# Kernel tuning notes

Hardware: AMD Instinct MI355X
Metric: run time of the kernel (lower is better)

## Reference

```python
import jax, jax.numpy as jnp
import numpy as np

N_NODES = 50000
N_EDGES = 1600000
NODE_DIM = 64
HID = 16


def setup_inputs() -> dict:
    key = jax.random.key(0)
    ks = jax.random.split(key, 12)
    f = lambda k, shape: (jax.random.normal(k, shape, dtype=jnp.float32) * 0.1)
    edge_index = jax.random.randint(ks[0], (2, N_EDGES), 0, N_NODES)
    return {
        "edge_index": edge_index,
        "node_emb": f(ks[1], (N_NODES, NODE_DIM)),
        "edge_emb": f(ks[2], (N_EDGES, HID)),
        "W1": f(ks[3], (NODE_DIM, HID)),
        "att_src1": f(ks[4], (HID,)),
        "att_dst1": f(ks[5], (HID,)),
        "b1": jnp.zeros((HID,), jnp.float32),
        "W2": f(ks[6], (HID, HID)),
        "att_src2": f(ks[7], (HID,)),
        "att_dst2": f(ks[8], (HID,)),
        "b2": jnp.zeros((HID,), jnp.float32),
        "Wm1": f(ks[9], (3 * HID, HID)),
        "bm1": jnp.zeros((HID,), jnp.float32),
        "Wm2": f(ks[10], (HID, 1)),
        "bm2": jnp.zeros((1,), jnp.float32),
    }


def gat_layer(x, src, dst, W, a_src, a_dst, b, num_nodes):
    # Single-head GATConv (PyG defaults): self-loops, leaky_relu(0.2), softmax over dst.
    h = x @ W  # [N, out]
    logits = jax.nn.leaky_relu((h @ a_src)[src] + (h @ a_dst)[dst], negative_slope=0.2)
    m = jax.ops.segment_max(logits, dst, num_segments=num_nodes)  # stable softmax
    e = jnp.exp(logits - jax.lax.stop_gradient(m)[dst])
    denom = jax.ops.segment_sum(e, dst, num_segments=num_nodes)
    coef = e / denom[dst]  # [E+N]
    out = jax.ops.segment_sum(coef[:, None] * h[src], dst, num_segments=num_nodes)
    return out + b


def reference(edge_index, node_emb, edge_emb, W1, att_src1, att_dst1, b1,
              W2, att_src2, att_dst2, b2, Wm1, bm1, Wm2, bm2):
    src, dst = edge_index[0], edge_index[1]
    num_nodes = node_emb.shape[0]
    loops = jnp.arange(num_nodes)
    src_f = jnp.concatenate([src, loops])  # GATConv add_self_loops=True
    dst_f = jnp.concatenate([dst, loops])

    x = node_emb
    for (W, a_s, a_d, b) in [(W1, att_src1, att_dst1, b1), (W2, att_src2, att_dst2, b2)]:
        x = gat_layer(x, src_f, dst_f, W, a_s, a_d, b, num_nodes)
        x = jax.nn.gelu(x, approximate=False)  # torch F.gelu default = exact erf
        # dropout omitted (eval mode)

    # Vectorized replacement of the per-edge Python loop:
    edge_repr = jnp.concatenate([x[src], x[dst], edge_emb], axis=1)  # [E, 3*HID]
    hmid = jax.nn.relu(edge_repr @ Wm1 + bm1)
    probs = jax.nn.sigmoid(hmid @ Wm2 + bm2)[:, 0]  # [E]
    return probs
```

## Files before the change

### kernel.cpp

```cpp
#include <hip/hip_runtime.h>
#include <math.h>

#define N_NODES 50000
#define N_EDGES 1600000
#define NODE_DIM 64
#define HID 16
#define BSZ 64
#define NBUCK ((N_NODES + BSZ - 1) / BSZ)
#define CAPB 2560
#define EPB 2048
#define APB 256
#define APPEND_BLOCKS ((N_EDGES + EPB - 1) / EPB)

typedef _Float16 h8 __attribute__((ext_vector_type(8)));

__global__ void append_kernel(const int* __restrict__ ei,
                              int* __restrict__ gcount,
                              unsigned int* __restrict__ blist) {
    __shared__ int lcount[NBUCK];
    __shared__ int gbase[NBUCK];
    __shared__ int loff[NBUCK];
    int t = threadIdx.x;
    for (int b = t; b < NBUCK; b += APB) { lcount[b] = 0; loff[b] = 0; }
    __syncthreads();
    long base = (long)blockIdx.x * EPB;
#pragma unroll
    for (int k = 0; k < EPB / APB; k++) {
        long i = base + k * APB + t;
        if (i < N_EDGES) atomicAdd(&lcount[ei[N_EDGES + i] >> 6], 1);
    }
    __syncthreads();
    for (int b = t; b < NBUCK; b += APB) {
        int c = lcount[b];
        gbase[b] = c ? atomicAdd(&gcount[b], c) : 0;
    }
    __syncthreads();
#pragma unroll
    for (int k = 0; k < EPB / APB; k++) {
        long i = base + k * APB + t;
        if (i < N_EDGES) {
            int s = ei[i], d = ei[N_EDGES + i];
            int b = d >> 6;
            int pos = gbase[b] + atomicAdd(&loff[b], 1);
            if (pos < CAPB)
                blist[(size_t)b * CAPB + pos] = ((unsigned)(d & 63) << 16) | (unsigned)s;
        }
    }
}

__global__ void sort_kernel(const int* __restrict__ gcount, const unsigned int* __restrict__ blist,
                            unsigned short* __restrict__ csr, int* __restrict__ dstbeg) {
    __shared__ int cnts[BSZ];
    __shared__ int sc[BSZ];
    __shared__ int off[BSZ];
    int b = blockIdx.x, t = threadIdx.x;
    if (t < BSZ) cnts[t] = 0;
    __syncthreads();
    int cnt = gcount[b]; if (cnt > CAPB) cnt = CAPB;
    const unsigned int* lp = blist + (size_t)b * CAPB;
    for (int k = t; k < cnt; k += APB) atomicAdd(&cnts[lp[k] >> 16], 1);
    __syncthreads();
    if (t < BSZ) sc[t] = cnts[t];
    __syncthreads();
    for (int o = 1; o < BSZ; o <<= 1) {
        int v = 0;
        if (t < BSZ && t >= o) v = sc[t - o];
        __syncthreads();
        if (t < BSZ) sc[t] += v;
        __syncthreads();
    }
    if (t < BSZ) {
        int beg = sc[t] - cnts[t];
        off[t] = beg;
        dstbeg[(b << 6) + t] = beg;
    }
    __syncthreads();
    for (int k = t; k < cnt; k += APB) {
        unsigned int r = lp[k];
        int pos = atomicAdd(&off[r >> 16], 1);
        csr[(size_t)b * CAPB + pos] = (unsigned short)(r & 0xFFFF);
    }
}

__global__ void node_h64(const float* __restrict__ x,
                         const float* __restrict__ W,
                         const float* __restrict__ a_src,
                         const float* __restrict__ a_dst,
                         float* __restrict__ h,
                         float* __restrict__ as_, float* __restrict__ ad_) {
    int t = threadIdx.x;
    int n = blockIdx.x * blockDim.x + t;
    if (n >= N_NODES) return;
    float acc[HID];
#pragma unroll
    for (int j = 0; j < HID; j++) acc[j] = 0.f;
    const float4* xr = (const float4*)(x + (size_t)n * NODE_DIM);
#pragma unroll
    for (int k4 = 0; k4 < NODE_DIM / 4; k4++) {
        float4 xv = xr[k4];
        const float* w0 = W + (k4 * 4) * HID;
#pragma unroll
        for (int j = 0; j < HID; j++)
            acc[j] += xv.x * w0[j] + xv.y * w0[HID + j] + xv.z * w0[2 * HID + j] + xv.w * w0[3 * HID + j];
    }
    float s = 0.f, d = 0.f;
#pragma unroll
    for (int j = 0; j < HID; j++) {
        h[(size_t)n * HID + j] = acc[j];
        s += acc[j] * a_src[j];
        d += acc[j] * a_dst[j];
    }
    as_[n] = s; ad_[n] = d;
}

__global__ void gather1_fused(const int* __restrict__ gcount, const int* __restrict__ dstbeg,
                              const unsigned short* __restrict__ csr,
                              const float* __restrict__ h,
                              const float* __restrict__ as_, const float* __restrict__ ad_,
                              const float* __restrict__ b,
                              const float* __restrict__ W2,
                              const float* __restrict__ a_src2,
                              const float* __restrict__ a_dst2,
                              float* __restrict__ h2out,
                              float* __restrict__ as2, float* __restrict__ ad2) {
    int t = threadIdx.x;
    int j = t & 15;
    int half = (t >> 4) & 1;
    float Wcol[HID];
#pragma unroll
    for (int k = 0; k < HID; k++) Wcol[k] = W2[k * HID + j];
    float a2j = a_src2[j], d2j = a_dst2[j], bj = b[j];
    int g = blockIdx.x * (blockDim.x >> 5) + (t >> 5);
    if (g >= N_NODES) return;
    int bk = g >> 6, dl = g & 63;
    int cnt_b = gcount[bk]; if (cnt_b > CAPB) cnt_b = CAPB;
    int beg = dstbeg[g];
    int end = (dl < 63) ? dstbeg[g + 1] : cnt_b;
    if (end > cnt_b) end = cnt_b;
    if (beg > end) beg = end;
    const unsigned short* row = csr + (size_t)bk * CAPB + beg;
    int cnt = end - beg;
    int ch = (cnt + 1) >> 1;
    int lo = half ? ch : 0;
    int hi = half ? cnt : ch;
    float adn = ad_[g];
    float acc = 0.f, den = 0.f;
    int k = lo;
    for (; k + 4 <= hi; k += 4) {
        int s0 = row[k], s1 = row[k + 1], s2 = row[k + 2], s3 = row[k + 3];
        float l0 = as_[s0] + adn, l1 = as_[s1] + adn;
        float l2 = as_[s2] + adn, l3 = as_[s3] + adn;
        l0 = l0 > 0.f ? l0 : 0.2f * l0;
        l1 = l1 > 0.f ? l1 : 0.2f * l1;
        l2 = l2 > 0.f ? l2 : 0.2f * l2;
        l3 = l3 > 0.f ? l3 : 0.2f * l3;
        float e0 = expf(l0), e1 = expf(l1), e2 = expf(l2), e3 = expf(l3);
        float h0 = h[(size_t)s0 * HID + j], h1 = h[(size_t)s1 * HID + j];
        float h2 = h[(size_t)s2 * HID + j], h3 = h[(size_t)s3 * HID + j];
        den += (e0 + e1) + (e2 + e3);
        acc += (e0 * h0 + e1 * h1) + (e2 * h2 + e3 * h3);
    }
    for (; k < hi; k++) {
        int s = row[k];
        float lg = as_[s] + adn;
        lg = lg > 0.f ? lg : 0.2f * lg;
        float e = expf(lg);
        den += e;
        acc += e * h[(size_t)s * HID + j];
    }
    acc += __shfl_xor(acc, 16, 32);
    den += __shfl_xor(den, 16, 32);
    float lg = as_[g] + adn;
    lg = lg > 0.f ? lg : 0.2f * lg;
    float e = expf(lg);
    den += e;
    acc += e * h[(size_t)g * HID + j];
    float v = acc / den + bj;
    v = 0.5f * v * (1.f + erff(v * 0.70710678118654752f));
    float acc2 = 0.f;
#pragma unroll
    for (int k2 = 0; k2 < HID; k2++) {
        float xk = __shfl(v, k2, 16);
        acc2 += xk * Wcol[k2];
    }
    float ps = acc2 * a2j, pd = acc2 * d2j;
#pragma unroll
    for (int o = 1; o < 16; o <<= 1) {
        ps += __shfl_xor(ps, o, 16);
        pd += __shfl_xor(pd, o, 16);
    }
    if (half == 0) {
        h2out[(size_t)g * HID + j] = acc2;
        if (j == 0) { as2[g] = ps; ad2[g] = pd; }
    }
}

__global__ void gather2_fused(const int* __restrict__ gcount, const int* __restrict__ dstbeg,
                              const unsigned short* __restrict__ csr,
                              const float* __restrict__ h,
                              const float* __restrict__ as_, const float* __restrict__ ad_,
                              const float* __restrict__ b,
                              const float* __restrict__ Wm1,
                              const float* __restrict__ bm1,
                              _Float16* __restrict__ A, _Float16* __restrict__ B) {
    int t = threadIdx.x;
    int j = t & 15;
    int half = (t >> 4) & 1;
    float WaC[HID], WbC[HID];
#pragma unroll
    for (int k = 0; k < HID; k++) {
        WaC[k] = Wm1[k * HID + j];
        WbC[k] = Wm1[HID * HID + k * HID + j];
    }
    float bj = b[j], b1j = bm1[j];
    int g = blockIdx.x * (blockDim.x >> 5) + (t >> 5);
    if (g >= N_NODES) return;
    int bk = g >> 6, dl = g & 63;
    int cnt_b = gcount[bk]; if (cnt_b > CAPB) cnt_b = CAPB;
    int beg = dstbeg[g];
    int end = (dl < 63) ? dstbeg[g + 1] : cnt_b;
    if (end > cnt_b) end = cnt_b;
    if (beg > end) beg = end;
    const unsigned short* row = csr + (size_t)bk * CAPB + beg;
    int cnt = end - beg;
    int ch = (cnt + 1) >> 1;
    int lo = half ? ch : 0;
    int hi = half ? cnt : ch;
    float adn = ad_[g];
    float acc = 0.f, den = 0.f;
    int k = lo;
    for (; k + 4 <= hi; k += 4) {
        int s0 = row[k], s1 = row[k + 1], s2 = row[k + 2], s3 = row[k + 3];
        float l0 = as_[s0] + adn, l1 = as_[s1] + adn;
        float l2 = as_[s2] + adn, l3 = as_[s3] + adn;
        l0 = l0 > 0.f ? l0 : 0.2f * l0;
        l1 = l1 > 0.f ? l1 : 0.2f * l1;
        l2 = l2 > 0.f ? l2 : 0.2f * l2;
        l3 = l3 > 0.f ? l3 : 0.2f * l3;
        float e0 = expf(l0), e1 = expf(l1), e2 = expf(l2), e3 = expf(l3);
        float h0 = h[(size_t)s0 * HID + j], h1 = h[(size_t)s1 * HID + j];
        float h2 = h[(size_t)s2 * HID + j], h3 = h[(size_t)s3 * HID + j];
        den += (e0 + e1) + (e2 + e3);
        acc += (e0 * h0 + e1 * h1) + (e2 * h2 + e3 * h3);
    }
    for (; k < hi; k++) {
        int s = row[k];
        float lg = as_[s] + adn;
        lg = lg > 0.f ? lg : 0.2f * lg;
        float e = expf(lg);
        den += e;
        acc += e * h[(size_t)s * HID + j];
    }
    acc += __shfl_xor(acc, 16, 32);
    den += __shfl_xor(den, 16, 32);
    float lg = as_[g] + adn;
    lg = lg > 0.f ? lg : 0.2f * lg;
    float e = expf(lg);
    den += e;
    acc += e * h[(size_t)g * HID + j];
    float v = acc / den + bj;
    v = 0.5f * v * (1.f + erff(v * 0.70710678118654752f));
    float accA = b1j, accB = 0.f;
#pragma unroll
    for (int k2 = 0; k2 < HID; k2++) {
        float xk = __shfl(v, k2, 16);
        accA += xk * WaC[k2];
        accB += xk * WbC[k2];
    }
    if (half == 0) {
        A[(size_t)g * HID + j] = (_Float16)accA;
        B[(size_t)g * HID + j] = (_Float16)accB;
    }
}

__global__ void edge_mlp(const int* __restrict__ ei,
                         const _Float16* __restrict__ A,
                         const _Float16* __restrict__ B,
                         const float* __restrict__ ee,
                         const float* __restrict__ Wm1,
                         const float* __restrict__ Wm2,
                         const float* __restrict__ bm2,
                         float* __restrict__ out) {
    int t = threadIdx.x;
    long i = (long)blockIdx.x * blockDim.x + t;
    if (i >= N_EDGES) return;
    int s = ei[i], d = ei[N_EDGES + i];
    const h8* Ap = (const h8*)(A + (size_t)s * HID);
    const h8* Bp = (const h8*)(B + (size_t)d * HID);
    h8 a0 = Ap[0], a1 = Ap[1];
    h8 b0 = Bp[0], b1 = Bp[1];
    const float4* ep = (const float4*)(ee + (size_t)i * HID);
    float4 e0 = ep[0], e1 = ep[1], e2 = ep[2], e3 = ep[3];
    float a[HID];
#pragma unroll
    for (int j = 0; j < 8; j++) {
        a[j]     = (float)a0[j] + (float)b0[j];
        a[8 + j] = (float)a1[j] + (float)b1[j];
    }
    float ev[HID];
    ev[0]  = e0.x; ev[1]  = e0.y; ev[2]  = e0.z; ev[3]  = e0.w;
    ev[4]  = e1.x; ev[5]  = e1.y; ev[6]  = e1.z; ev[7]  = e1.w;
    ev[8]  = e2.x; ev[9]  = e2.y; ev[10] = e2.z; ev[11] = e2.w;
    ev[12] = e3.x; ev[13] = e3.y; ev[14] = e3.z; ev[15] = e3.w;
    const float4* W4 = (const float4*)(Wm1 + 2 * HID * HID);
#pragma unroll
    for (int k = 0; k < HID; k++) {
        float e1v = ev[k];
        float4 w0 = W4[k * 4 + 0], w1 = W4[k * 4 + 1], w2 = W4[k * 4 + 2], w3 = W4[k * 4 + 3];
        a[0]  += e1v * w0.x; a[1]  += e1v * w0.y; a[2]  += e1v * w0.z; a[3]  += e1v * w0.w;
        a[4]  += e1v * w1.x; a[5]  += e1v * w1.y; a[6]  += e1v * w1.z; a[7]  += e1v * w1.w;
        a[8]  += e1v * w2.x; a[9]  += e1v * w2.y; a[10] += e1v * w2.z; a[11] += e1v * w2.w;
        a[12] += e1v * w3.x; a[13] += e1v * w3.y; a[14] += e1v * w3.z; a[15] += e1v * w3.w;
    }
    float o = bm2[0];
#pragma unroll
    for (int j = 0; j < HID; j++) o += fmaxf(a[j], 0.f) * Wm2[j];
    out[i] = 1.f / (1.f + expf(-o));
}

extern "C" void kernel_launch(void* const* d_in, const int* in_sizes, int n_in,
                              void* d_out, int out_size, void* d_ws, size_t ws_size,
                              hipStream_t stream) {
    const int*   ei       = (const int*)d_in[0];
    const float* node_emb = (const float*)d_in[1];
    const float* edge_emb = (const float*)d_in[2];
    const float* W1       = (const float*)d_in[3];
    const float* att_src1 = (const float*)d_in[4];
    const float* att_dst1 = (const float*)d_in[5];
    const float* b1       = (const float*)d_in[6];
    const float* W2       = (const float*)d_in[7];
    const float* att_src2 = (const float*)d_in[8];
    const float* att_dst2 = (const float*)d_in[9];
    const float* b2       = (const float*)d_in[10];
    const float* Wm1      = (const float*)d_in[11];
    const float* bm1      = (const float*)d_in[12];
    const float* Wm2      = (const float*)d_in[13];
    const float* bm2      = (const float*)d_in[14];
    float* out            = (float*)d_out;

    char* w = (char*)d_ws;
    float*          h      = (float*)w;          w += (size_t)N_NODES * HID * 4;
    float*          h2     = (float*)w;          w += (size_t)N_NODES * HID * 4;
    float*          as_    = (float*)w;          w += (size_t)N_NODES * 4;
    float*          ad_    = (float*)w;          w += (size_t)N_NODES * 4;
    int*            gcount = (int*)w;            w += (size_t)NBUCK * 4;
    unsigned int*   blist  = (unsigned int*)w;   w += (size_t)NBUCK * CAPB * 4;
    unsigned short* csr    = (unsigned short*)w; w += (size_t)NBUCK * CAPB * 2;
    int*            dstbeg = (int*)w;            w += (size_t)NBUCK * BSZ * 4;

    _Float16* Anode = (_Float16*)blist;
    _Float16* Bnode = Anode + (size_t)N_NODES * HID;
    float*    as2   = (float*)(Bnode + (size_t)N_NODES * HID);
    float*    ad2   = as2 + N_NODES;

    const int BT = 256;
    int nblk_node = (N_NODES + BT - 1) / BT;
    int nblk_E    = (N_EDGES + BT - 1) / BT;
    int nblk_g32  = (N_NODES + (BT >> 5) - 1) / (BT >> 5);

    hipMemsetAsync(gcount, 0, (size_t)NBUCK * sizeof(int), stream);
    append_kernel<<<APPEND_BLOCKS, APB, 0, stream>>>(ei, gcount, blist);
    sort_kernel<<<NBUCK, APB, 0, stream>>>(gcount, blist, csr, dstbeg);

    node_h64<<<nblk_node, BT, 0, stream>>>(node_emb, W1, att_src1, att_dst1, h, as_, ad_);
    gather1_fused<<<nblk_g32, BT, 0, stream>>>(gcount, dstbeg, csr, h, as_, ad_, b1,
                                               W2, att_src2, att_dst2, h2, as2, ad2);

    gather2_fused<<<nblk_g32, BT, 0, stream>>>(gcount, dstbeg, csr, h2, as2, ad2, b2,
                                               Wm1, bm1, Anode, Bnode);

    edge_mlp<<<nblk_E, BT, 0, stream>>>(ei, Anode, Bnode, edge_emb, Wm1, Wm2, bm2, out);
}
```

Measured before the change: 355.1 us.

## Precompute fp16 edge softmax weights and gather fp16 features with 16-lane groups

Adds an exp_kernel that computes each edge's attention exponent once, packs it as fp16 bits with the source index into a 32-bit record, and writes the per-node denominator. The gather kernels then read these records coalesced, broadcast them via shuffles, and gather fp16 node features using one 16-lane group per node instead of two halves of 32 lanes. The aim is to remove the redundant per-lane exp and as_ lookups and to halve gather bandwidth, at the cost of two extra launches, an extra pass over the edges, and fp16 rounding of the attention weights and features.

New measurement: 353.6 us. Within noise of the previous version (-0.4%).

```diff
diff --git a/kernel.cpp b/kernel.cpp
--- a/kernel.cpp
+++ b/kernel.cpp
@@ -1,5 +1,6 @@
 #include <hip/hip_runtime.h>
 #include <math.h>
+#include <string.h>
 
 #define N_NODES 50000
 #define N_EDGES 1600000
@@ -14,6 +15,19 @@
 
 typedef _Float16 h8 __attribute__((ext_vector_type(8)));
 
+__device__ __forceinline__ unsigned short half_bits(float a) {
+    _Float16 ha = (_Float16)a;
+    unsigned short ua;
+    __builtin_memcpy(&ua, &ha, 2);
+    return ua;
+}
+__device__ __forceinline__ float bits_half(unsigned int ub) {
+    unsigned short us = (unsigned short)ub;
+    _Float16 hv;
+    __builtin_memcpy(&hv, &us, 2);
+    return (float)hv;
+}
+
 __global__ void append_kernel(const int* __restrict__ ei,
                               int* __restrict__ gcount,
                               unsigned int* __restrict__ blist) {
@@ -86,7 +100,7 @@
                          const float* __restrict__ W,
                          const float* __restrict__ a_src,
                          const float* __restrict__ a_dst,
-                         float* __restrict__ h,
+                         _Float16* __restrict__ h16,
                          float* __restrict__ as_, float* __restrict__ ad_) {
     int t = threadIdx.x;
     int n = blockIdx.x * blockDim.x + t;
@@ -106,31 +120,24 @@
     float s = 0.f, d = 0.f;
 #pragma unroll
     for (int j = 0; j < HID; j++) {
-        h[(size_t)n * HID + j] = acc[j];
         s += acc[j] * a_src[j];
         d += acc[j] * a_dst[j];
     }
+    h8 hv0, hv1;
+#pragma unroll
+    for (int j = 0; j < 8; j++) { hv0[j] = (_Float16)acc[j]; hv1[j] = (_Float16)acc[8 + j]; }
+    h8* hp = (h8*)(h16 + (size_t)n * HID);
+    hp[0] = hv0; hp[1] = hv1;
     as_[n] = s; ad_[n] = d;
 }
 
-__global__ void gather1_fused(const int* __restrict__ gcount, const int* __restrict__ dstbeg,
-                              const unsigned short* __restrict__ csr,
-                              const float* __restrict__ h,
-                              const float* __restrict__ as_, const float* __restrict__ ad_,
-                              const float* __restrict__ b,
-                              const float* __restrict__ W2,
-                              const float* __restrict__ a_src2,
-                              const float* __restrict__ a_dst2,
-                              float* __restrict__ h2out,
-                              float* __restrict__ as2, float* __restrict__ ad2) {
+__global__ void exp_kernel(const int* __restrict__ gcount, const int* __restrict__ dstbeg,
+                           const unsigned short* __restrict__ csr,
+                           const float* __restrict__ as_, const float* __restrict__ ad_,
+                           unsigned int* __restrict__ crec, float* __restrict__ den) {
     int t = threadIdx.x;
     int j = t & 15;
-    int half = (t >> 4) & 1;
-    float Wcol[HID];
-#pragma unroll
-    for (int k = 0; k < HID; k++) Wcol[k] = W2[k * HID + j];
-    float a2j = a_src2[j], d2j = a_dst2[j], bj = b[j];
-    int g = blockIdx.x * (blockDim.x >> 5) + (t >> 5);
+    int g = blockIdx.x * (blockDim.x >> 4) + (t >> 4);
     if (g >= N_NODES) return;
     int bk = g >> 6, dl = g & 63;
     int cnt_b = gcount[bk]; if (cnt_b > CAPB) cnt_b = CAPB;
@@ -138,82 +145,72 @@
     int end = (dl < 63) ? dstbeg[g + 1] : cnt_b;
     if (end > cnt_b) end = cnt_b;
     if (beg > end) beg = end;
-    const unsigned short* row = csr + (size_t)bk * CAPB + beg;
-    int cnt = end - beg;
-    int ch = (cnt + 1) >> 1;
-    int lo = half ? ch : 0;
-    int hi = half ? cnt : ch;
+    const unsigned short* row = csr + (size_t)bk * CAPB;
+    unsigned int* cr = crec + (size_t)bk * CAPB;
     float adn = ad_[g];
-    float acc = 0.f, den = 0.f;
-    int k = lo;
-    for (; k + 4 <= hi; k += 4) {
-        int s0 = row[k], s1 = row[k + 1], s2 = row[k + 2], s3 = row[k + 3];
-        float l0 = as_[s0] + adn, l1 = as_[s1] + adn;
-        float l2 = as_[s2] + adn, l3 = as_[s3] + adn;
-        l0 = l0 > 0.f ? l0 : 0.2f * l0;
-        l1 = l1 > 0.f ? l1 : 0.2f * l1;
-        l2 = l2 > 0.f ? l2 : 0.2f * l2;
-        l3 = l3 > 0.f ? l3 : 0.2f * l3;
-        float e0 = expf(l0), e1 = expf(l1), e2 = expf(l2), e3 = expf(l3);
-        float h0 = h[(size_t)s0 * HID + j], h1 = h[(size_t)s1 * HID + j];
-        float h2 = h[(size_t)s2 * HID + j], h3 = h[(size_t)s3 * HID + j];
-        den += (e0 + e1) + (e2 + e3);
-        acc += (e0 * h0 + e1 * h1) + (e2 * h2 + e3 * h3);
-    }
-    for (; k < hi; k++) {
+    float dsum = 0.f;
+    for (int k = beg + j; k < end; k += 16) {
         int s = row[k];
         float lg = as_[s] + adn;
         lg = lg > 0.f ? lg : 0.2f * lg;
         float e = expf(lg);
-        den += e;
-        acc += e * h[(size_t)s * HID + j];
-    }
-    acc += __shfl_xor(acc, 16, 32);
-    den += __shfl_xor(den, 16, 32);
-    float lg = as_[g] + adn;
-    lg = lg > 0.f ? lg : 0.2f * lg;
-    float e = expf(lg);
-    den += e;
-    acc += e * h[(size_t)g * HID + j];
-    float v = acc / den + bj;
-    v = 0.5f * v * (1.f + erff(v * 0.70710678118654752f));
-    float acc2 = 0.f;
-#pragma unroll
-    for (int k2 = 0; k2 < HID; k2++) {
-        float xk = __shfl(v, k2, 16);
-        acc2 += xk * Wcol[k2];
-    }
-    float ps = acc2 * a2j, pd = acc2 * d2j;
-#pragma unroll
-    for (int o = 1; o < 16; o <<= 1) {
-        ps += __shfl_xor(ps, o, 16);
-        pd += __shfl_xor(pd, o, 16);
-    }
-    if (half == 0) {
-        h2out[(size_t)g * HID + j] = acc2;
-        if (j == 0) { as2[g] = ps; ad2[g] = pd; }
-    }
-}
-
-__global__ void gather2_fused(const int* __restrict__ gcount, const int* __restrict__ dstbeg,
-                              const unsigned short* __restrict__ csr,
-                              const float* __restrict__ h,
+        unsigned short eb = half_bits(e);
+        dsum += bits_half(eb);
+        cr[k] = ((unsigned)eb << 16) | (unsigned)s;
+    }
+#pragma unroll
+    for (int o = 1; o < 16; o <<= 1) dsum += __shfl_xor(dsum, o, 16);
+    if (j == 0) den[g] = dsum;
+}
+
+__device__ __forceinline__ void gather_core(
+        const unsigned int* __restrict__ cr, int beg, int end, int j,
+        const _Float16* __restrict__ h16, float& acc) {
+    int base = beg;
+    for (; base + 16 <= end; base += 16) {
+        unsigned int c = cr[base + j];
+#pragma unroll
+        for (int e = 0; e < 16; e += 4) {
+            unsigned int c0 = (unsigned)__shfl((int)c, e, 16);
+            unsigned int c1 = (unsigned)__shfl((int)c, e + 1, 16);
+            unsigned int c2 = (unsigned)__shfl((int)c, e + 2, 16);
+            unsigned int c3 = (unsigned)__shfl((int)c, e + 3, 16);
+            float h0 = (float)h16[(size_t)(c0 & 0xffffu) * HID + j];
+            float h1 = (float)h16[(size_t)(c1 & 0xffffu) * HID + j];
+            float h2 = (float)h16[(size_t)(c2 & 0xffffu) * HID + j];
+            float h3 = (float)h16[(size_t)(c3 & 0xffffu) * HID + j];
+            acc += bits_half(c0 >> 16) * h0 + bits_half(c1 >> 16) * h1
+                 + bits_half(c2 >> 16) * h2 + bits_half(c3 >> 16) * h3;
+        }
+    }
+    int nb = end - base;
+    if (nb > 0) {
+        unsigned int c = (base + j < end) ? cr[base + j] : 0u;
+        for (int e = 0; e < nb; e++) {
+            unsigned int ce = (unsigned)__shfl((int)c, e, 16);
+            acc += bits_half(ce >> 16) * (float)h16[(size_t)(ce & 0xffffu) * HID + j];
+        }
+    }
+}
+
+__global__ void gather1_fused(const int* __restrict__ gcount, const int* __restrict__ dstbeg,
+                              const unsigned int* __restrict__ crec,
+                              const _Float16* __restrict__ h1,
                               const float* __restrict__ as_, const float* __restrict__ ad_,
+                              const float* __restrict__ den,
                               const float* __restrict__ b,
-                              const float* __restrict__ Wm1,
-                              const float* __restrict__ bm1,
-                              _Float16* __restrict__ A, _Float16* __restrict__ B) {
+                              const float* __restrict__ W2,
+                              const float* __restrict__ a_src2,
+                              const float* __restrict__ a_dst2,
+                              _Float16* __restrict__ h2,
+                              float* __restrict__ as2, float* __restrict__ ad2) {
     int t = threadIdx.x;
     int j = t & 15;
-    int half = (t >> 4) & 1;
-    float WaC[HID], WbC[HID];
-#pragma unroll
-    for (int k = 0; k < HID; k++) {
-        WaC[k] = Wm1[k * HID + j];
-        WbC[k] = Wm1[HID * HID + k * HID + j];
-    }
-    float bj = b[j], b1j = bm1[j];
-    int g = blockIdx.x * (blockDim.x >> 5) + (t >> 5);
+    float Wcol[HID];
+#pragma unroll
+    for (int k = 0; k < HID; k++) Wcol[k] = W2[k * HID + j];
+    float a2j = a_src2[j], d2j = a_dst2[j], bj = b[j];
+    int g = blockIdx.x * (blockDim.x >> 4) + (t >> 4);
     if (g >= N_NODES) return;
     int bk = g >> 6, dl = g & 63;
     int cnt_b = gcount[bk]; if (cnt_b > CAPB) cnt_b = CAPB;
@@ -221,44 +218,69 @@
     int end = (dl < 63) ? dstbeg[g + 1] : cnt_b;
     if (end > cnt_b) end = cnt_b;
     if (beg > end) beg = end;
-    const unsigned short* row = csr + (size_t)bk * CAPB + beg;
-    int cnt = end - beg;
-    int ch = (cnt + 1) >> 1;
-    int lo = half ? ch : 0;
-    int hi = half ? cnt : ch;
+    const unsigned int* cr = crec + (size_t)bk * CAPB;
+    float acc = 0.f;
+    gather_core(cr, beg, end, j, h1, acc);
     float adn = ad_[g];
-    float acc = 0.f, den = 0.f;
-    int k = lo;
-    for (; k + 4 <= hi; k += 4) {
-        int s0 = row[k], s1 = row[k + 1], s2 = row[k + 2], s3 = row[k + 3];
-        float l0 = as_[s0] + adn, l1 = as_[s1] + adn;
-        float l2 = as_[s2] + adn, l3 = as_[s3] + adn;
-        l0 = l0 > 0.f ? l0 : 0.2f * l0;
-        l1 = l1 > 0.f ? l1 : 0.2f * l1;
-        l2 = l2 > 0.f ? l2 : 0.2f * l2;
-        l3 = l3 > 0.f ? l3 : 0.2f * l3;
-        float e0 = expf(l0), e1 = expf(l1), e2 = expf(l2), e3 = expf(l3);
-        float h0 = h[(size_t)s0 * HID + j], h1 = h[(size_t)s1 * HID + j];
-        float h2 = h[(size_t)s2 * HID + j], h3 = h[(size_t)s3 * HID + j];
-        den += (e0 + e1) + (e2 + e3);
-        acc += (e0 * h0 + e1 * h1) + (e2 * h2 + e3 * h3);
-    }
-    for (; k < hi; k++) {
-        int s = row[k];
-        float lg = as_[s] + adn;
-        lg = lg > 0.f ? lg : 0.2f * lg;
-        float e = expf(lg);
-        den += e;
-        acc += e * h[(size_t)s * HID + j];
-    }
-    acc += __shfl_xor(acc, 16, 32);
-    den += __shfl_xor(den, 16, 32);
     float lg = as_[g] + adn;
     lg = lg > 0.f ? lg : 0.2f * lg;
-    float e = expf(lg);
-    den += e;
-    acc += e * h[(size_t)g * HID + j];
-    float v = acc / den + bj;
+    float es = expf(lg);
+    float dent = den[g] + es;
+    acc += es * (float)h1[(size_t)g * HID + j];
+    float v = acc / dent + bj;
+    v = 0.5f * v * (1.f + erff(v * 0.70710678118654752f));
+    float acc2 = 0.f;
+#pragma unroll
+    for (int k2 = 0; k2 < HID; k2++) {
+        float xk = __shfl(v, k2, 16);
+        acc2 += xk * Wcol[k2];
+    }
+    float ps = acc2 * a2j, pd = acc2 * d2j;
+#pragma unroll
+    for (int o = 1; o < 16; o <<= 1) {
+        ps += __shfl_xor(ps, o, 16);
+        pd += __shfl_xor(pd, o, 16);
+    }
+    h2[(size_t)g * HID + j] = (_Float16)acc2;
+    if (j == 0) { as2[g] = ps; ad2[g] = pd; }
+}
+
+__global__ void gather2_fused(const int* __restrict__ gcount, const int* __restrict__ dstbeg,
+                              const unsigned int* __restrict__ crec,
+                              const _Float16* __restrict__ h2,
+                              const float* __restrict__ as_, const float* __restrict__ ad_,
+                              const float* __restrict__ den,
+                              const float* __restrict__ b,
+                              const float* __restrict__ Wm1,
+                              const float* __restrict__ bm1,
+                              _Float16* __restrict__ A, _Float16* __restrict__ B) {
+    int t = threadIdx.x;
+    int j = t & 15;
+    float WaC[HID], WbC[HID];
+#pragma unroll
+    for (int k = 0; k < HID; k++) {
+        WaC[k] = Wm1[k * HID + j];
+        WbC[k] = Wm1[HID * HID + k * HID + j];
+    }
+    float bj = b[j], b1j = bm1[j];
+    int g = blockIdx.x * (blockDim.x >> 4) + (t >> 4);
+    if (g >= N_NODES) return;
+    int bk = g >> 6, dl = g & 63;
+    int cnt_b = gcount[bk]; if (cnt_b > CAPB) cnt_b = CAPB;
+    int beg = dstbeg[g];
+    int end = (dl < 63) ? dstbeg[g + 1] : cnt_b;
+    if (end > cnt_b) end = cnt_b;
+    if (beg > end) beg = end;
+    const unsigned int* cr = crec + (size_t)bk * CAPB;
+    float acc = 0.f;
+    gather_core(cr, beg, end, j, h2, acc);
+    float adn = ad_[g];
+    float lg = as_[g] + adn;
+    lg = lg > 0.f ? lg : 0.2f * lg;
+    float es = expf(lg);
+    float dent = den[g] + es;
+    acc += es * (float)h2[(size_t)g * HID + j];
+    float v = acc / dent + bj;
     v = 0.5f * v * (1.f + erff(v * 0.70710678118654752f));
     float accA = b1j, accB = 0.f;
 #pragma unroll
@@ -267,10 +289,8 @@
         accA += xk * WaC[k2];
         accB += xk * WbC[k2];
     }
-    if (half == 0) {
-        A[(size_t)g * HID + j] = (_Float16)accA;
-        B[(size_t)g * HID + j] = (_Float16)accB;
-    }
+    A[(size_t)g * HID + j] = (_Float16)accA;
+    B[(size_t)g * HID + j] = (_Float16)accB;
 }
 
 __global__ void edge_mlp(const int* __restrict__ ei,
@@ -339,35 +359,39 @@
     float* out            = (float*)d_out;
 
     char* w = (char*)d_ws;
-    float*          h      = (float*)w;          w += (size_t)N_NODES * HID * 4;
-    float*          h2     = (float*)w;          w += (size_t)N_NODES * HID * 4;
-    float*          as_    = (float*)w;          w += (size_t)N_NODES * 4;
-    float*          ad_    = (float*)w;          w += (size_t)N_NODES * 4;
+    _Float16*       h1     = (_Float16*)w;       w += (size_t)N_NODES * HID * 2;
+    _Float16*       h2     = (_Float16*)w;       w += (size_t)N_NODES * HID * 2;
+    _Float16*       Anode  = (_Float16*)w;       w += (size_t)N_NODES * HID * 2;
+    _Float16*       Bnode  = (_Float16*)w;       w += (size_t)N_NODES * HID * 2;
+    float*          as1    = (float*)w;          w += (size_t)N_NODES * 4;
+    float*          ad1    = (float*)w;          w += (size_t)N_NODES * 4;
+    float*          as2    = (float*)w;          w += (size_t)N_NODES * 4;
+    float*          ad2    = (float*)w;          w += (size_t)N_NODES * 4;
+    float*          den    = (float*)w;          w += (size_t)N_NODES * 4;
     int*            gcount = (int*)w;            w += (size_t)NBUCK * 4;
     unsigned int*   blist  = (unsigned int*)w;   w += (size_t)NBUCK * CAPB * 4;
     unsigned short* csr    = (unsigned short*)w; w += (size_t)NBUCK * CAPB * 2;
     int*            dstbeg = (int*)w;            w += (size_t)NBUCK * BSZ * 4;
 
-    _Float16* Anode = (_Float16*)blist;
-    _Float16* Bnode = Anode + (size_t)N_NODES * HID;
-    float*    as2   = (float*)(Bnode + (size_t)N_NODES * HID);
-    float*    ad2   = as2 + N_NODES;
+    unsigned int* crec = blist;
 
     const int BT = 256;
     int nblk_node = (N_NODES + BT - 1) / BT;
     int nblk_E    = (N_EDGES + BT - 1) / BT;
-    int nblk_g32  = (N_NODES + (BT >> 5) - 1) / (BT >> 5);
+    int nblk_g    = (N_NODES * HID + BT - 1) / BT;
 
     hipMemsetAsync(gcount, 0, (size_t)NBUCK * sizeof(int), stream);
     append_kernel<<<APPEND_BLOCKS, APB, 0, stream>>>(ei, gcount, blist);
     sort_kernel<<<NBUCK, APB, 0, stream>>>(gcount, blist, csr, dstbeg);
 
-    node_h64<<<nblk_node, BT, 0, stream>>>(node_emb, W1, att_src1, att_dst1, h, as_, ad_);
-    gather1_fused<<<nblk_g32, BT, 0, stream>>>(gcount, dstbeg, csr, h, as_, ad_, b1,
-                                               W2, att_src2, att_dst2, h2, as2, ad2);
-
-    gather2_fused<<<nblk_g32, BT, 0, stream>>>(gcount, dstbeg, csr, h2, as2, ad2, b2,
-                                               Wm1, bm1, Anode, Bnode);
+    node_h64<<<nblk_node, BT, 0, stream>>>(node_emb, W1, att_src1, att_dst1, h1, as1, ad1);
+    exp_kernel<<<nblk_g, BT, 0, stream>>>(gcount, dstbeg, csr, as1, ad1, crec, den);
+    gather1_fused<<<nblk_g, BT, 0, stream>>>(gcount, dstbeg, crec, h1, as1, ad1, den, b1,
+                                             W2, att_src2, att_dst2, h2, as2, ad2);
+
+    exp_kernel<<<nblk_g, BT, 0, stream>>>(gcount, dstbeg, csr, as2, ad2, crec, den);
+    gather2_fused<<<nblk_g, BT, 0, stream>>>(gcount, dstbeg, crec, h2, as2, ad2, den, b2,
+                                             Wm1, bm1, Anode, Bnode);
 
     edge_mlp<<<nblk_E, BT, 0, stream>>>(ei, Anode, Bnode, edge_emb, Wm1, Wm2, bm2, out);
 }
```

## Store node features in fp16, use 16 lanes per node, fold memset

Applied to the files above, without the earlier changes.

Node feature buffers h1 and h2 are now stored as fp16, which halves the bytes touched by the random per-edge gathers in both GAT aggregation kernels. Each destination node is now handled by 16 lanes instead of 32 split into halves, so the cross-half shuffle reduction goes away and twice as many blocks are launched. The bucket-count memset is folded into the first node kernel, which now runs before the edge append, and the workspace no longer aliases blist. Fp16 storage of hidden features adds rounding error, and dropping the edge split lengthens each thread's serial loop.

Measured after the change: 340.3 us. -4.2%, faster.

```diff
diff --git a/kernel.cpp b/kernel.cpp
--- a/kernel.cpp
+++ b/kernel.cpp
@@ -1,5 +1,6 @@
 #include <hip/hip_runtime.h>
 #include <math.h>
+#include <string.h>
 
 #define N_NODES 50000
 #define N_EDGES 1600000
@@ -86,10 +87,12 @@
                          const float* __restrict__ W,
                          const float* __restrict__ a_src,
                          const float* __restrict__ a_dst,
-                         float* __restrict__ h,
-                         float* __restrict__ as_, float* __restrict__ ad_) {
+                         _Float16* __restrict__ h16,
+                         float* __restrict__ as_, float* __restrict__ ad_,
+                         int* __restrict__ gcount) {
     int t = threadIdx.x;
     int n = blockIdx.x * blockDim.x + t;
+    if (n < NBUCK) gcount[n] = 0;
     if (n >= N_NODES) return;
     float acc[HID];
 #pragma unroll
@@ -106,31 +109,65 @@
     float s = 0.f, d = 0.f;
 #pragma unroll
     for (int j = 0; j < HID; j++) {
-        h[(size_t)n * HID + j] = acc[j];
         s += acc[j] * a_src[j];
         d += acc[j] * a_dst[j];
     }
+    h8 hv0, hv1;
+#pragma unroll
+    for (int j = 0; j < 8; j++) { hv0[j] = (_Float16)acc[j]; hv1[j] = (_Float16)acc[8 + j]; }
+    h8* hp = (h8*)(h16 + (size_t)n * HID);
+    hp[0] = hv0; hp[1] = hv1;
     as_[n] = s; ad_[n] = d;
+}
+
+__device__ __forceinline__ void gather_core(
+        const unsigned short* __restrict__ row, int cnt, int j,
+        const _Float16* __restrict__ h16, const float* __restrict__ as_, float adn,
+        float& acc, float& den) {
+    int k = 0;
+    for (; k + 4 <= cnt; k += 4) {
+        int s0 = row[k], s1 = row[k + 1], s2 = row[k + 2], s3 = row[k + 3];
+        float l0 = as_[s0] + adn, l1 = as_[s1] + adn;
+        float l2 = as_[s2] + adn, l3 = as_[s3] + adn;
+        l0 = l0 > 0.f ? l0 : 0.2f * l0;
+        l1 = l1 > 0.f ? l1 : 0.2f * l1;
+        l2 = l2 > 0.f ? l2 : 0.2f * l2;
+        l3 = l3 > 0.f ? l3 : 0.2f * l3;
+        float e0 = expf(l0), e1 = expf(l1), e2 = expf(l2), e3 = expf(l3);
+        float h0 = (float)h16[(size_t)s0 * HID + j];
+        float h1 = (float)h16[(size_t)s1 * HID + j];
+        float h2 = (float)h16[(size_t)s2 * HID + j];
+        float h3 = (float)h16[(size_t)s3 * HID + j];
+        den += (e0 + e1) + (e2 + e3);
+        acc += (e0 * h0 + e1 * h1) + (e2 * h2 + e3 * h3);
+    }
+    for (; k < cnt; k++) {
+        int s = row[k];
+        float lg = as_[s] + adn;
+        lg = lg > 0.f ? lg : 0.2f * lg;
+        float e = expf(lg);
+        den += e;
+        acc += e * (float)h16[(size_t)s * HID + j];
+    }
 }
 
 __global__ void gather1_fused(const int* __restrict__ gcount, const int* __restrict__ dstbeg,
                               const unsigned short* __restrict__ csr,
-                              const float* __restrict__ h,
+                              const _Float16* __restrict__ h1,
                               const float* __restrict__ as_, const float* __restrict__ ad_,
                               const float* __restrict__ b,
                               const float* __restrict__ W2,
                               const float* __restrict__ a_src2,
                               const float* __restrict__ a_dst2,
-                              float* __restrict__ h2out,
+                              _Float16* __restrict__ h2,
                               float* __restrict__ as2, float* __restrict__ ad2) {
     int t = threadIdx.x;
     int j = t & 15;
-    int half = (t >> 4) & 1;
     float Wcol[HID];
 #pragma unroll
     for (int k = 0; k < HID; k++) Wcol[k] = W2[k * HID + j];
     float a2j = a_src2[j], d2j = a_dst2[j], bj = b[j];
-    int g = blockIdx.x * (blockDim.x >> 5) + (t >> 5);
+    int g = blockIdx.x * (blockDim.x >> 4) + (t >> 4);
     if (g >= N_NODES) return;
     int bk = g >> 6, dl = g & 63;
     int cnt_b = gcount[bk]; if (cnt_b > CAPB) cnt_b = CAPB;
@@ -139,42 +176,14 @@
     if (end > cnt_b) end = cnt_b;
     if (beg > end) beg = end;
     const unsigned short* row = csr + (size_t)bk * CAPB + beg;
-    int cnt = end - beg;
-    int ch = (cnt + 1) >> 1;
-    int lo = half ? ch : 0;
-    int hi = half ? cnt : ch;
     float adn = ad_[g];
     float acc = 0.f, den = 0.f;
-    int k = lo;
-    for (; k + 4 <= hi; k += 4) {
-        int s0 = row[k], s1 = row[k + 1], s2 = row[k + 2], s3 = row[k + 3];
-        float l0 = as_[s0] + adn, l1 = as_[s1] + adn;
-        float l2 = as_[s2] + adn, l3 = as_[s3] + adn;
-        l0 = l0 > 0.f ? l0 : 0.2f * l0;
-        l1 = l1 > 0.f ? l1 : 0.2f * l1;
-        l2 = l2 > 0.f ? l2 : 0.2f * l2;
-        l3 = l3 > 0.f ? l3 : 0.2f * l3;
-        float e0 = expf(l0), e1 = expf(l1), e2 = expf(l2), e3 = expf(l3);
-        float h0 = h[(size_t)s0 * HID + j], h1 = h[(size_t)s1 * HID + j];
-        float h2 = h[(size_t)s2 * HID + j], h3 = h[(size_t)s3 * HID + j];
-        den += (e0 + e1) + (e2 + e3);
-        acc += (e0 * h0 + e1 * h1) + (e2 * h2 + e3 * h3);
-    }
-    for (; k < hi; k++) {
-        int s = row[k];
-        float lg = as_[s] + adn;
-        lg = lg > 0.f ? lg : 0.2f * lg;
-        float e = expf(lg);
-        den += e;
-        acc += e * h[(size_t)s * HID + j];
-    }
-    acc += __shfl_xor(acc, 16, 32);
-    den += __shfl_xor(den, 16, 32);
+    gather_core(row, end - beg, j, h1, as_, adn, acc, den);
     float lg = as_[g] + adn;
     lg = lg > 0.f ? lg : 0.2f * lg;
     float e = expf(lg);
     den += e;
-    acc += e * h[(size_t)g * HID + j];
+    acc += e * (float)h1[(size_t)g * HID + j];
     float v = acc / den + bj;
     v = 0.5f * v * (1.f + erff(v * 0.70710678118654752f));
     float acc2 = 0.f;
@@ -189,15 +198,13 @@
         ps += __shfl_xor(ps, o, 16);
         pd += __shfl_xor(pd, o, 16);
     }
-    if (half == 0) {
-        h2out[(size_t)g * HID + j] = acc2;
-        if (j == 0) { as2[g] = ps; ad2[g] = pd; }
-    }
+    h2[(size_t)g * HID + j] = (_Float16)acc2;
+    if (j == 0) { as2[g] = ps; ad2[g] = pd; }
 }
 
 __global__ void gather2_fused(const int* __restrict__ gcount, const int* __restrict__ dstbeg,
                               const unsigned short* __restrict__ csr,
-                              const float* __restrict__ h,
+                              const _Float16* __restrict__ h2,
                               const float* __restrict__ as_, const float* __restrict__ ad_,
                               const float* __restrict__ b,
                               const float* __restrict__ Wm1,
@@ -205,7 +212,6 @@
                               _Float16* __restrict__ A, _Float16* __restrict__ B) {
     int t = threadIdx.x;
     int j = t & 15;
-    int half = (t >> 4) & 1;
     float WaC[HID], WbC[HID];
 #pragma unroll
     for (int k = 0; k < HID; k++) {
@@ -213,7 +219,7 @@
         WbC[k] = Wm1[HID * HID + k * HID + j];
     }
     float bj = b[j], b1j = bm1[j];
-    int g = blockIdx.x * (blockDim.x >> 5) + (t >> 5);
+    int g = blockIdx.x * (blockDim.x >> 4) + (t >> 4);
     if (g >= N_NODES) return;
     int bk = g >> 6, dl = g & 63;
     int cnt_b = gcount[bk]; if (cnt_b > CAPB) cnt_b = CAPB;
@@ -222,42 +228,14 @@
     if (end > cnt_b) end = cnt_b;
     if (beg > end) beg = end;
     const unsigned short* row = csr + (size_t)bk * CAPB + beg;
-    int cnt = end - beg;
-    int ch = (cnt + 1) >> 1;
-    int lo = half ? ch : 0;
-    int hi = half ? cnt : ch;
     float adn = ad_[g];
     float acc = 0.f, den = 0.f;
-    int k = lo;
-    for (; k + 4 <= hi; k += 4) {
-        int s0 = row[k], s1 = row[k + 1], s2 = row[k + 2], s3 = row[k + 3];
-        float l0 = as_[s0] + adn, l1 = as_[s1] + adn;
-        float l2 = as_[s2] + adn, l3 = as_[s3] + adn;
-        l0 = l0 > 0.f ? l0 : 0.2f * l0;
-        l1 = l1 > 0.f ? l1 : 0.2f * l1;
-        l2 = l2 > 0.f ? l2 : 0.2f * l2;
-        l3 = l3 > 0.f ? l3 : 0.2f * l3;
-        float e0 = expf(l0), e1 = expf(l1), e2 = expf(l2), e3 = expf(l3);
-        float h0 = h[(size_t)s0 * HID + j], h1 = h[(size_t)s1 * HID + j];
-        float h2 = h[(size_t)s2 * HID + j], h3 = h[(size_t)s3 * HID + j];
-        den += (e0 + e1) + (e2 + e3);
-        acc += (e0 * h0 + e1 * h1) + (e2 * h2 + e3 * h3);
-    }
-    for (; k < hi; k++) {
-        int s = row[k];
-        float lg = as_[s] + adn;
-        lg = lg > 0.f ? lg : 0.2f * lg;
-        float e = expf(lg);
-        den += e;
-        acc += e * h[(size_t)s * HID + j];
-    }
-    acc += __shfl_xor(acc, 16, 32);
-    den += __shfl_xor(den, 16, 32);
+    gather_core(row, end - beg, j, h2, as_, adn, acc, den);
     float lg = as_[g] + adn;
     lg = lg > 0.f ? lg : 0.2f * lg;
     float e = expf(lg);
     den += e;
-    acc += e * h[(size_t)g * HID + j];
+    acc += e * (float)h2[(size_t)g * HID + j];
     float v = acc / den + bj;
     v = 0.5f * v * (1.f + erff(v * 0.70710678118654752f));
     float accA = b1j, accB = 0.f;
@@ -267,10 +245,8 @@
         accA += xk * WaC[k2];
         accB += xk * WbC[k2];
     }
-    if (half == 0) {
-        A[(size_t)g * HID + j] = (_Float16)accA;
-        B[(size_t)g * HID + j] = (_Float16)accB;
-    }
+    A[(size_t)g * HID + j] = (_Float16)accA;
+    B[(size_t)g * HID + j] = (_Float16)accB;
 }
 
 __global__ void edge_mlp(const int* __restrict__ ei,
@@ -339,35 +315,33 @@
     float* out            = (float*)d_out;
 
     char* w = (char*)d_ws;
-    float*          h      = (float*)w;          w += (size_t)N_NODES * HID * 4;
-    float*          h2     = (float*)w;          w += (size_t)N_NODES * HID * 4;
-    float*          as_    = (float*)w;          w += (size_t)N_NODES * 4;
-    float*          ad_    = (float*)w;          w += (size_t)N_NODES * 4;
+    _Float16*       h1     = (_Float16*)w;       w += (size_t)N_NODES * HID * 2;
+    _Float16*       h2     = (_Float16*)w;       w += (size_t)N_NODES * HID * 2;
+    _Float16*       Anode  = (_Float16*)w;       w += (size_t)N_NODES * HID * 2;
+    _Float16*       Bnode  = (_Float16*)w;       w += (size_t)N_NODES * HID * 2;
+    float*          as1    = (float*)w;          w += (size_t)N_NODES * 4;
+    float*          ad1    = (float*)w;          w += (size_t)N_NODES * 4;
+    float*          as2    = (float*)w;          w += (size_t)N_NODES * 4;
+    float*          ad2    = (float*)w;          w += (size_t)N_NODES * 4;
     int*            gcount = (int*)w;            w += (size_t)NBUCK * 4;
     unsigned int*   blist  = (unsigned int*)w;   w += (size_t)NBUCK * CAPB * 4;
     unsigned short* csr    = (unsigned short*)w; w += (size_t)NBUCK * CAPB * 2;
     int*            dstbeg = (int*)w;            w += (size_t)NBUCK * BSZ * 4;
 
-    _Float16* Anode = (_Float16*)blist;
-    _Float16* Bnode = Anode + (size_t)N_NODES * HID;
-    float*    as2   = (float*)(Bnode + (size_t)N_NODES * HID);
-    float*    ad2   = as2 + N_NODES;
-
     const int BT = 256;
     int nblk_node = (N_NODES + BT - 1) / BT;
     int nblk_E    = (N_EDGES + BT - 1) / BT;
-    int nblk_g32  = (N_NODES + (BT >> 5) - 1) / (BT >> 5);
-
-    hipMemsetAsync(gcount, 0, (size_t)NBUCK * sizeof(int), stream);
+    int nblk_g    = (N_NODES * HID + BT - 1) / BT;
+
+    node_h64<<<nblk_node, BT, 0, stream>>>(node_emb, W1, att_src1, att_dst1,
+                                           h1, as1, ad1, gcount);
     append_kernel<<<APPEND_BLOCKS, APB, 0, stream>>>(ei, gcount, blist);
     sort_kernel<<<NBUCK, APB, 0, stream>>>(gcount, blist, csr, dstbeg);
 
-    node_h64<<<nblk_node, BT, 0, stream>>>(node_emb, W1, att_src1, att_dst1, h, as_, ad_);
-    gather1_fused<<<nblk_g32, BT, 0, stream>>>(gcount, dstbeg, csr, h, as_, ad_, b1,
-                                               W2, att_src2, att_dst2, h2, as2, ad2);
-
-    gather2_fused<<<nblk_g32, BT, 0, stream>>>(gcount, dstbeg, csr, h2, as2, ad2, b2,
-                                               Wm1, bm1, Anode, Bnode);
+    gather1_fused<<<nblk_g, BT, 0, stream>>>(gcount, dstbeg, csr, h1, as1, ad1, b1,
+                                             W2, att_src2, att_dst2, h2, as2, ad2);
+    gather2_fused<<<nblk_g, BT, 0, stream>>>(gcount, dstbeg, csr, h2, as2, ad2, b2,
+                                             Wm1, bm1, Anode, Bnode);
 
     edge_mlp<<<nblk_E, BT, 0, stream>>>(ei, Anode, Bnode, edge_emb, Wm1, Wm2, bm2, out);
 }
```
